# Kernel tuning notes

Hardware: AMD Instinct MI355X
Metric: run time of the kernel (lower is better)

## Reference

```python
import jax, jax.numpy as jnp
import numpy as np
from jax import lax

B, T, I, H = 8192, 512, 3, 25  # batch, seq_len, input_size, hidden_size


def setup_inputs() -> dict:
    key = jax.random.key(0)
    ks = jax.random.split(key, 4)
    x = jax.random.normal(ks[0], (B, T, I), dtype=jnp.float32)
    # xavier-uniform-ish scale for w_ih, orthogonal-ish (plain normal here) for w_hh
    w_ih = jax.random.normal(ks[1], (4 * H, I), dtype=jnp.float32) * 0.5
    w_hh = jax.random.normal(ks[2], (4 * H, H), dtype=jnp.float32) * 0.2
    b_ih = jnp.zeros((4 * H,), dtype=jnp.float32)
    # PyTorch init in module: forget-gate bias (second quarter) set to 1 on each bias
    b_ih = b_ih.at[H:2 * H].set(1.0)
    b_hh = jnp.zeros((4 * H,), dtype=jnp.float32)
    b_hh = b_hh.at[H:2 * H].set(1.0)
    w_lin = jax.random.normal(ks[3], (1, H), dtype=jnp.float32) * 0.3
    b_lin = jnp.zeros((1,), dtype=jnp.float32)
    return {"x": x, "w_ih": w_ih, "w_hh": w_hh, "b_ih": b_ih, "b_hh": b_hh,
            "w_lin": w_lin, "b_lin": b_lin}


def _lstm_last_h(x, w_ih, w_hh, b_ih, b_hh):
    # x: [B, T, I]; returns final hidden state h_T: [B, H]
    b = b_ih + b_hh  # [4H]
    xT = jnp.swapaxes(x, 0, 1)  # [T, B, I]

    def step(carry, x_t):
        h, c = carry
        gates = x_t @ w_ih.T + h @ w_hh.T + b  # [B, 4H]
        i, f, g, o = jnp.split(gates, 4, axis=-1)  # PyTorch gate order i,f,g,o
        i = jax.nn.sigmoid(i)
        f = jax.nn.sigmoid(f)
        g = jnp.tanh(g)
        o = jax.nn.sigmoid(o)
        c = f * c + i * g
        h = o * jnp.tanh(c)
        return (h, c), None

    h0 = jnp.zeros((x.shape[0], w_hh.shape[1]), dtype=x.dtype)
    (h, _), _ = lax.scan(step, (h0, h0), xT)
    return h


def reference(x, w_ih, w_hh, b_ih, b_hh, w_lin, b_lin):
    h_last = _lstm_last_h(x, w_ih, w_hh, b_ih, b_hh)  # [B, H]
    return h_last @ w_lin.T + b_lin  # [B, 1]
```

## Files before the change

kernel.cpp:

```cpp
#include <hip/hip_runtime.h>
#include <hip/hip_bf16.h>


#define TSTEPS 512
#define ISZ 3
#define HSZ 25

typedef __attribute__((ext_vector_type(8))) short bf16x8;
typedef __attribute__((ext_vector_type(4))) float f32x4;
typedef __attribute__((ext_vector_type(4))) int i32x4;
typedef __attribute__((ext_vector_type(2))) float v2f;

__device__ __forceinline__ unsigned short bf16_bits(float v) {
    return __builtin_bit_cast(unsigned short, __float2bfloat16(v));
}
__device__ __forceinline__ unsigned int pack_bf16(float lo, float hi) {
    return ((unsigned int)bf16_bits(hi) << 16) | (unsigned int)bf16_bits(lo);
}
__device__ __forceinline__ v2f rcp2(v2f v) {
    return (v2f){__builtin_amdgcn_rcpf(v.x), __builtin_amdgcn_rcpf(v.y)};
}

__global__ __launch_bounds__(512, 2) void lstm_mfma(
    const float* __restrict__ x,
    const float* __restrict__ w_ih,
    const float* __restrict__ w_hh,
    const float* __restrict__ b_ih,
    const float* __restrict__ b_hh,
    const float* __restrict__ w_lin,
    const float* __restrict__ b_lin,
    float* __restrict__ out)
{
    __shared__ short hb[2][2][768];
    __shared__ float outred[8][16];

    const int tid  = threadIdx.x;
    const int w    = tid >> 6;
    const int lane = tid & 63;
    const int n    = lane & 15;
    const int q    = lane >> 4;
    const int ch   = w >> 2;
    const int wv   = w & 3;
    const int b0   = blockIdx.x * 32;

    const float K1 = 1.442695040888963f;
    const float K2 = 2.885390081777927f;

    if (tid < 384) ((int4*)hb)[tid] = (int4){0, 0, 0, 0};

    bf16x8 afA, afB;
    {
        const int g = n & 3, us = n >> 2;
        const int uA = 4 * wv + us;
        const int uB = 4 * (wv + 4) + us;
        #pragma unroll
        for (int j = 0; j < 8; ++j) {
            const int k = q * 8 + j;
            float vA = 0.f, vB = 0.f;
            {
                const int orow = g * HSZ + uA;
                if (k < ISZ)            vA = w_ih[orow * ISZ + k];
                else if (k == ISZ)      vA = b_ih[orow] + b_hh[orow];
                else if (k < 4 + HSZ)   vA = w_hh[orow * HSZ + (k - 4)];
                vA *= (g == 2) ? -K2 : -K1;
            }
            if (uB < HSZ) {
                const int orow = g * HSZ + uB;
                if (k < ISZ)            vB = w_ih[orow * ISZ + k];
                else if (k == ISZ)      vB = b_ih[orow] + b_hh[orow];
                else if (k < 4 + HSZ)   vB = w_hh[orow * HSZ + (k - 4)];
                vB *= (g == 2) ? -K2 : -K1;
            }
            afA[j] = (short)bf16_bits(vA);
            afB[j] = (short)bf16_bits(vB);
        }
    }

    const int uwA = 4 * wv + q;
    const int uwB = 4 * (wv + 4) + q;
    const int kwA = uwA + 4, kwB = uwB + 4;
    const int woffA = (kwA >> 3) * 128 + n * 8 + (kwA & 7);
    const int woffB = (kwB >> 3) * 128 + n * 8 + (kwB & 7);
    const int rdoff = lane * 8;

    v2f c = {0.f, 0.f}, h = {0.f, 0.f};

    const float* __restrict__ xg =
        x + (size_t)(b0 + ch * 16 + n) * (TSTEPS * ISZ);
    float4 a0 = ((const float4*)xg)[0];
    float4 a1 = ((const float4*)xg)[1];
    float4 a2 = ((const float4*)xg)[2];

    __syncthreads();

    auto step = [&](int rp, float x0, float x1, float x2) {
        bf16x8 frag = *(const bf16x8*)&hb[ch][rp][rdoff];
        i32x4 fi = __builtin_bit_cast(i32x4, frag);
        const int px0 = (int)pack_bf16(x0, x1);
        const int px1 = (int)pack_bf16(x2, 1.0f);
        fi[0] = (q == 0) ? px0 : fi[0];
        fi[1] = (q == 0) ? px1 : fi[1];
        frag = __builtin_bit_cast(bf16x8, fi);

        const f32x4 zc = {0.f, 0.f, 0.f, 0.f};
        const f32x4 aA = __builtin_amdgcn_mfma_f32_16x16x32_bf16(afA, frag, zc, 0, 0, 0);
        const f32x4 aB = __builtin_amdgcn_mfma_f32_16x16x32_bf16(afB, frag, zc, 0, 0, 0);

        const v2f e0 = {__builtin_amdgcn_exp2f(aA[0]), __builtin_amdgcn_exp2f(aB[0])};
        const v2f e1 = {__builtin_amdgcn_exp2f(aA[1]), __builtin_amdgcn_exp2f(aB[1])};
        const v2f e2 = {__builtin_amdgcn_exp2f(fminf(aA[2], 126.f)),
                        __builtin_amdgcn_exp2f(fminf(aB[2], 126.f))};
        const v2f e3 = {__builtin_amdgcn_exp2f(aA[3]), __builtin_amdgcn_exp2f(aB[3])};
        const v2f one = {1.f, 1.f};
        const v2f s0 = e0 + one, s1 = e1 + one, s2 = e2 + one, m2 = one - e2;
        const v2f p02 = s0 * s2;
        const v2f num = c * p02 + m2 * s1;
        const v2f den = p02 * s1;
        c = num * rcp2(den);
        const v2f ec = {__builtin_amdgcn_exp2f(fminf(-K2 * c.x, 126.f)),
                        __builtin_amdgcn_exp2f(fminf(-K2 * c.y, 126.f))};
        const v2f hden = (e3 + one) * (ec + one);
        h = (one - ec) * rcp2(hden);

        const int wp = rp ^ 1;
        hb[ch][wp][woffA] = (short)bf16_bits(h.x);
        hb[ch][wp][woffB] = (short)bf16_bits(h.y);
        asm volatile("s_waitcnt lgkmcnt(0)" ::: "memory");
        __builtin_amdgcn_s_barrier();
    };

    #pragma unroll 1
    for (int g = 0; g < 128; g += 2) {
        const float4* __restrict__ p1 =
            (const float4*)(xg + (size_t)((g + 1 < 128 ? g + 1 : 127) * 12));
        const float4 n0 = p1[0], n1 = p1[1], n2 = p1[2];
        step(0, a0.x, a0.y, a0.z);
        step(1, a0.w, a1.x, a1.y);
        step(0, a1.z, a1.w, a2.x);
        step(1, a2.y, a2.z, a2.w);
        const float4* __restrict__ p2 =
            (const float4*)(xg + (size_t)((g + 2 < 128 ? g + 2 : 127) * 12));
        a0 = p2[0]; a1 = p2[1]; a2 = p2[2];
        step(0, n0.x, n0.y, n0.z);
        step(1, n0.w, n1.x, n1.y);
        step(0, n1.z, n1.w, n2.x);
        step(1, n2.y, n2.z, n2.w);
    }

    const float wlA = (uwA < HSZ) ? w_lin[uwA] : 0.f;
    const float wlB = (uwB < HSZ) ? w_lin[uwB] : 0.f;
    float v = wlA * h.x + wlB * h.y;
    v += __shfl_xor(v, 16);
    v += __shfl_xor(v, 32);
    if (lane < 16) outred[w][lane] = v;
    __syncthreads();
    if (tid < 32) {
        const int c2 = tid >> 4;
        float s = b_lin[0];
        #pragma unroll
        for (int k2 = 0; k2 < 4; ++k2) s += outred[c2 * 4 + k2][tid & 15];
        out[b0 + tid] = s;
    }
}

extern "C" void kernel_launch(void* const* d_in, const int* in_sizes, int n_in,
                              void* d_out, int out_size, void* d_ws, size_t ws_size,
                              hipStream_t stream) {
    const float* x     = (const float*)d_in[0];
    const float* w_ih  = (const float*)d_in[1];
    const float* w_hh  = (const float*)d_in[2];
    const float* b_ih  = (const float*)d_in[3];
    const float* b_hh  = (const float*)d_in[4];
    const float* w_lin = (const float*)d_in[5];
    const float* b_lin = (const float*)d_in[6];
    float* out = (float*)d_out;

    lstm_mfma<<<8192 / 32, 512, 0, stream>>>(x, w_ih, w_hh, b_ih, b_hh,
                                             w_lin, b_lin, out);
}
```

Baseline: 270.4 us.

## Ping-pong the two LSTM chains so one runs MFMA while the other runs activations

Each step is split into an MFMA phase and an activation phase separated by barriers. The two batch chains in a block are offset by half a step, so on each SIMD one chain's matrix multiply can overlap the other chain's transcendental math. Because reads and writes are now separated by barriers, the h buffer is single instead of double-buffered. Launch bounds are relaxed to one block per CU. The cost is twice as many block-wide barriers per timestep, which may lengthen the serial per-step latency.

New measurement: 302.8 us. 12.0% more time.

```diff
diff --git a/kernel.cpp b/kernel.cpp
--- a/kernel.cpp
+++ b/kernel.cpp
@@ -21,7 +21,7 @@
     return (v2f){__builtin_amdgcn_rcpf(v.x), __builtin_amdgcn_rcpf(v.y)};
 }
 
-__global__ __launch_bounds__(512, 2) void lstm_mfma(
+__global__ __launch_bounds__(512, 1) void lstm_mfma(
     const float* __restrict__ x,
     const float* __restrict__ w_ih,
     const float* __restrict__ w_hh,
@@ -31,7 +31,7 @@
     const float* __restrict__ b_lin,
     float* __restrict__ out)
 {
-    __shared__ short hb[2][2][768];
+    __shared__ short hb[2][768];
     __shared__ float outred[8][16];
 
     const int tid  = threadIdx.x;
@@ -46,7 +46,7 @@
     const float K1 = 1.442695040888963f;
     const float K2 = 2.885390081777927f;
 
-    if (tid < 384) ((int4*)hb)[tid] = (int4){0, 0, 0, 0};
+    if (tid < 192) ((int4*)hb)[tid] = (int4){0, 0, 0, 0};
 
     bf16x8 afA, afB;
     {
@@ -84,6 +84,8 @@
     const int rdoff = lane * 8;
 
     v2f c = {0.f, 0.f}, h = {0.f, 0.f};
+    f32x4 accA = {0.f, 0.f, 0.f, 0.f};
+    f32x4 accB = {0.f, 0.f, 0.f, 0.f};
 
     const float* __restrict__ xg =
         x + (size_t)(b0 + ch * 16 + n) * (TSTEPS * ISZ);
@@ -93,24 +95,25 @@
 
     __syncthreads();
 
-    auto step = [&](int rp, float x0, float x1, float x2) {
-        bf16x8 frag = *(const bf16x8*)&hb[ch][rp][rdoff];
+    auto mfmaP = [&](float x0, float x1, float x2) {
+        bf16x8 frag = *(const bf16x8*)&hb[ch][rdoff];
         i32x4 fi = __builtin_bit_cast(i32x4, frag);
         const int px0 = (int)pack_bf16(x0, x1);
         const int px1 = (int)pack_bf16(x2, 1.0f);
         fi[0] = (q == 0) ? px0 : fi[0];
         fi[1] = (q == 0) ? px1 : fi[1];
         frag = __builtin_bit_cast(bf16x8, fi);
-
         const f32x4 zc = {0.f, 0.f, 0.f, 0.f};
-        const f32x4 aA = __builtin_amdgcn_mfma_f32_16x16x32_bf16(afA, frag, zc, 0, 0, 0);
-        const f32x4 aB = __builtin_amdgcn_mfma_f32_16x16x32_bf16(afB, frag, zc, 0, 0, 0);
-
-        const v2f e0 = {__builtin_amdgcn_exp2f(aA[0]), __builtin_amdgcn_exp2f(aB[0])};
-        const v2f e1 = {__builtin_amdgcn_exp2f(aA[1]), __builtin_amdgcn_exp2f(aB[1])};
-        const v2f e2 = {__builtin_amdgcn_exp2f(fminf(aA[2], 126.f)),
-                        __builtin_amdgcn_exp2f(fminf(aB[2], 126.f))};
-        const v2f e3 = {__builtin_amdgcn_exp2f(aA[3]), __builtin_amdgcn_exp2f(aB[3])};
+        accA = __builtin_amdgcn_mfma_f32_16x16x32_bf16(afA, frag, zc, 0, 0, 0);
+        accB = __builtin_amdgcn_mfma_f32_16x16x32_bf16(afB, frag, zc, 0, 0, 0);
+    };
+
+    auto actsP = [&]() {
+        const v2f e0 = {__builtin_amdgcn_exp2f(accA[0]), __builtin_amdgcn_exp2f(accB[0])};
+        const v2f e1 = {__builtin_amdgcn_exp2f(accA[1]), __builtin_amdgcn_exp2f(accB[1])};
+        const v2f e2 = {__builtin_amdgcn_exp2f(fminf(accA[2], 126.f)),
+                        __builtin_amdgcn_exp2f(fminf(accB[2], 126.f))};
+        const v2f e3 = {__builtin_amdgcn_exp2f(accA[3]), __builtin_amdgcn_exp2f(accB[3])};
         const v2f one = {1.f, 1.f};
         const v2f s0 = e0 + one, s1 = e1 + one, s2 = e2 + one, m2 = one - e2;
         const v2f p02 = s0 * s2;
@@ -121,30 +124,52 @@
                         __builtin_amdgcn_exp2f(fminf(-K2 * c.y, 126.f))};
         const v2f hden = (e3 + one) * (ec + one);
         h = (one - ec) * rcp2(hden);
-
-        const int wp = rp ^ 1;
-        hb[ch][wp][woffA] = (short)bf16_bits(h.x);
-        hb[ch][wp][woffB] = (short)bf16_bits(h.y);
+        hb[ch][woffA] = (short)bf16_bits(h.x);
+        hb[ch][woffB] = (short)bf16_bits(h.y);
+    };
+
+    auto bar = [&]() {
         asm volatile("s_waitcnt lgkmcnt(0)" ::: "memory");
         __builtin_amdgcn_s_barrier();
     };
 
-    #pragma unroll 1
-    for (int g = 0; g < 128; g += 2) {
-        const float4* __restrict__ p1 =
-            (const float4*)(xg + (size_t)((g + 1 < 128 ? g + 1 : 127) * 12));
-        const float4 n0 = p1[0], n1 = p1[1], n2 = p1[2];
-        step(0, a0.x, a0.y, a0.z);
-        step(1, a0.w, a1.x, a1.y);
-        step(0, a1.z, a1.w, a2.x);
-        step(1, a2.y, a2.z, a2.w);
-        const float4* __restrict__ p2 =
-            (const float4*)(xg + (size_t)((g + 2 < 128 ? g + 2 : 127) * 12));
-        a0 = p2[0]; a1 = p2[1]; a2 = p2[2];
-        step(0, n0.x, n0.y, n0.z);
-        step(1, n0.w, n1.x, n1.y);
-        step(0, n1.z, n1.w, n2.x);
-        step(1, n2.y, n2.z, n2.w);
+    if (ch == 0) {
+        #pragma unroll 1
+        for (int g = 0; g < 128; g += 2) {
+            const int gp1 = (g + 1 < 128) ? g + 1 : 127;
+            const float4* __restrict__ p1 = (const float4*)(xg + (size_t)gp1 * 12);
+            const float4 n0 = p1[0], n1 = p1[1], n2 = p1[2];
+            mfmaP(a0.x, a0.y, a0.z); bar(); actsP(); bar();
+            mfmaP(a0.w, a1.x, a1.y); bar(); actsP(); bar();
+            mfmaP(a1.z, a1.w, a2.x); bar(); actsP(); bar();
+            mfmaP(a2.y, a2.z, a2.w); bar(); actsP(); bar();
+            const int gp2 = (g + 2 < 128) ? g + 2 : 127;
+            const float4* __restrict__ p2 = (const float4*)(xg + (size_t)gp2 * 12);
+            a0 = p2[0]; a1 = p2[1]; a2 = p2[2];
+            mfmaP(n0.x, n0.y, n0.z); bar(); actsP(); bar();
+            mfmaP(n0.w, n1.x, n1.y); bar(); actsP(); bar();
+            mfmaP(n1.z, n1.w, n2.x); bar(); actsP(); bar();
+            mfmaP(n2.y, n2.z, n2.w); bar(); actsP(); bar();
+        }
+    } else {
+        #pragma unroll 1
+        for (int g = 0; g < 128; g += 2) {
+            const int gp1 = (g + 1 < 128) ? g + 1 : 127;
+            const float4* __restrict__ p1 = (const float4*)(xg + (size_t)gp1 * 12);
+            const float4 n0 = p1[0], n1 = p1[1], n2 = p1[2];
+            actsP(); bar(); mfmaP(a0.x, a0.y, a0.z); bar();
+            actsP(); bar(); mfmaP(a0.w, a1.x, a1.y); bar();
+            actsP(); bar(); mfmaP(a1.z, a1.w, a2.x); bar();
+            actsP(); bar(); mfmaP(a2.y, a2.z, a2.w); bar();
+            const int gp2 = (g + 2 < 128) ? g + 2 : 127;
+            const float4* __restrict__ p2 = (const float4*)(xg + (size_t)gp2 * 12);
+            a0 = p2[0]; a1 = p2[1]; a2 = p2[2];
+            actsP(); bar(); mfmaP(n0.x, n0.y, n0.z); bar();
+            actsP(); bar(); mfmaP(n0.w, n1.x, n1.y); bar();
+            actsP(); bar(); mfmaP(n1.z, n1.w, n2.x); bar();
+            actsP(); bar(); mfmaP(n2.y, n2.z, n2.w); bar();
+        }
+        actsP();
     }
 
     const float wlA = (uwA < HSZ) ? w_lin[uwA] : 0.f;
@@ -155,11 +180,11 @@
     if (lane < 16) outred[w][lane] = v;
     __syncthreads();
     if (tid < 32) {
-        const int c2 = tid >> 4;
+        const int c2 = tid >> 4, nn = tid & 15;
         float s = b_lin[0];
         #pragma unroll
-        for (int k2 = 0; k2 < 4; ++k2) s += outred[c2 * 4 + k2][tid & 15];
-        out[b0 + tid] = s;
+        for (int k2 = 0; k2 < 4; ++k2) s += outred[c2 * 4 + k2][nn];
+        out[b0 + c2 * 16 + nn] = s;
     }
 }
 
```
